# Kernel optimization log

Measured on AMD Instinct MI355X. Metric: run time of the kernel, lower is better.

## Reference

```python
import jax, jax.numpy as jnp
import numpy as np

N, E, IN, ED, H, C = 50000, 800000, 128, 32, 4, 32
HC = H * C
SCALE = 1.0 / float(np.sqrt(C))


def _seg_softmax(t, idx, n):
    # t: [E, H], idx: [E] target-node ids -> per-segment softmax over incoming edges
    m = jax.ops.segment_max(t, idx, num_segments=n)
    m = jnp.where(jnp.isfinite(m), m, 0.0)
    e = jnp.exp(t - m[idx])
    z = jax.ops.segment_sum(e, idx, num_segments=n)
    return e / (z[idx] + 1e-16)


def setup_inputs() -> dict:
    key = jax.random.key(0)
    ks = jax.random.split(key, 26)
    w = lambda k, shape: (jax.random.normal(k, shape, jnp.float32) * 0.05)
    return {
        "x": jax.random.normal(ks[0], (N, IN), jnp.float32),
        "edge_index": jax.random.randint(ks[1], (2, E), 0, N),
        "edge_attr": jax.random.normal(ks[2], (E, ED), jnp.float32),
        # DifferentialGraphAttention params (dual QK groups + lambda)
        "Wq1": w(ks[3], (HC, IN)), "Wq2": w(ks[4], (HC, IN)),
        "Wk1": w(ks[5], (HC, IN)), "Wk2": w(ks[6], (HC, IN)),
        "Wvd": w(ks[7], (HC, IN)),
        "Wkr1": w(ks[8], (HC, ED)), "Wkr2": w(ks[9], (HC, ED)),
        "Wvrd": w(ks[10], (HC, ED)),
        "Woutd": w(ks[11], (HC, HC)),
        "lam": jnp.float32(0.8),
        # RelationActivationAttention params
        "Wqa": w(ks[12], (HC, IN)), "Wka": w(ks[13], (HC, IN)), "Wva": w(ks[14], (HC, IN)),
        "Wkra": w(ks[15], (HC, ED)), "Wvra": w(ks[16], (HC, ED)),
        "Wouta": w(ks[17], (HC, HC)),
        # Hybrid fusion params
        "Wproj": w(ks[18], (HC, 2 * HC)), "bproj": jnp.zeros((HC,), jnp.float32),
        "Win": w(ks[19], (HC, IN)), "b_in": jnp.zeros((HC,), jnp.float32),
        "rms_w": jnp.ones((HC,), jnp.float32),
    }


def reference(x, edge_index, edge_attr, Wq1, Wq2, Wk1, Wk2, Wvd, Wkr1, Wkr2, Wvrd,
              Woutd, lam, Wqa, Wka, Wva, Wkra, Wvra, Wouta, Wproj, bproj, Win, b_in,
              rms_w):
    src, dst = edge_index[0], edge_index[1]

    def nproj(W):  # [N, HC] -> [N, H, C]
        return (x @ W.T).reshape(N, H, C)

    def eproj(W):  # [E, HC] -> [E, H, C]
        return (edge_attr @ W.T).reshape(E, H, C)

    # ---- differential relation aggregation branch ----
    Q1, Q2, K1, K2, Vd = nproj(Wq1), nproj(Wq2), nproj(Wk1), nproj(Wk2), nproj(Wvd)
    t1 = jnp.sum(Q1[dst] * (K1[src] + eproj(Wkr1)), axis=-1) * SCALE  # [E, H]
    t2 = jnp.sum(Q2[dst] * (K2[src] + eproj(Wkr2)), axis=-1) * SCALE
    a_diff = _seg_softmax(t1, dst, N) - lam * _seg_softmax(t2, dst, N)
    msg_d = (Vd[src] + eproj(Wvrd)) * a_diff[..., None]               # [E, H, C]
    h_aggr = jax.ops.segment_sum(msg_d, dst, num_segments=N).reshape(N, HC) @ Woutd.T

    # ---- relation activation branch ----
    Qa, Ka, Va = nproj(Wqa), nproj(Wka), nproj(Wva)
    ta = jnp.sum(Qa[dst] * (Ka[src] + eproj(Wkra)), axis=-1) * SCALE  # [E, H]
    a_act = _seg_softmax(ta, dst, N)
    msg_a = (Va[src] + eproj(Wvra)) * a_act[..., None]
    h_actv = jax.ops.segment_sum(msg_a, dst, num_segments=N).reshape(N, HC) @ Wouta.T

    # ---- hybrid fusion + residual + RMSNorm ----
    h = jnp.concatenate([h_aggr, h_actv], axis=-1) @ Wproj.T + bproj
    h = h + (x @ Win.T + b_in)
    h = h * jax.lax.rsqrt(jnp.mean(h * h, axis=-1, keepdims=True) + 1e-6) * rms_w
    return h
```

## Files before the change

kernel.cpp:

```cpp
#include <hip/hip_runtime.h>

typedef unsigned short u16;
typedef unsigned int   u32;
typedef _Float16 half8 __attribute__((ext_vector_type(8)));
typedef _Float16 half2v __attribute__((ext_vector_type(2)));
typedef float    f32x4 __attribute__((ext_vector_type(4)));
typedef unsigned int u32x4 __attribute__((ext_vector_type(4)));
typedef int      i32x2 __attribute__((ext_vector_type(2)));

#define NN 50000
#define EE 800000
#define SCALE 0.17677669529663687f
#define NB 49

#define O_WNODET   0ul
#define O_WFT      393216ul
#define O_WF1      524288ul
#define O_WF3      589824ul
#define O_HIST     655360ul
#define O_BSUM     855360ul
#define O_BOFF     855616ul
#define O_OFF      856064ul
#define O_CUR      1056768ul
#define O_PERM     1257472ul
#define O_NODEQ    7657472ul
#define O_NODEKV   97257472ul
#define O_G        161257472ul

__device__ __forceinline__ float fin(float x){
  return (x == x && fabsf(x) < 3e38f) ? x : 0.f;
}
__device__ __forceinline__ u32 packh(float a, float b){
  union{ u32 u; _Float16 h[2]; } cv; cv.h[0]=(_Float16)a; cv.h[1]=(_Float16)b; return cv.u;
}
union H2U { u32 u; half2v h; };
__device__ __forceinline__ half2v h2(u32 u){ H2U c; c.u=u; return c.h; }

__device__ __forceinline__ u32x4 ntl4(const u32* p){
  return __builtin_nontemporal_load((const u32x4*)p);
}
__device__ __forceinline__ f32x4 ntlf4(const float* p){
  return __builtin_nontemporal_load((const f32x4*)p);
}
__device__ __forceinline__ i32x2 ntl2(const i32x2* p){
  return __builtin_nontemporal_load(p);
}

__global__ __launch_bounds__(256) void xcast(const float* __restrict__ x,
                                             _Float16* __restrict__ xh,
                                             int* __restrict__ hist, int* __restrict__ cur)
{
  int i = blockIdx.x*256 + threadIdx.x;
  if (i < NN){ hist[i] = 0; cur[i] = 0; }
  size_t b = (size_t)i * 8;
  float4 v0 = *(const float4*)(x + b);
  float4 v1 = *(const float4*)(x + b + 4);
  half8 h;
  h[0]=(_Float16)v0.x; h[1]=(_Float16)v0.y; h[2]=(_Float16)v0.z; h[3]=(_Float16)v0.w;
  h[4]=(_Float16)v1.x; h[5]=(_Float16)v1.y; h[6]=(_Float16)v1.z; h[7]=(_Float16)v1.w;
  *(half8*)(xh + b) = h;
}

__global__ __launch_bounds__(256) void prep1(
    const float* __restrict__ Wq1, const float* __restrict__ Wq2, const float* __restrict__ Wqa,
    const float* __restrict__ Wk1, const float* __restrict__ Wk2, const float* __restrict__ Wka,
    const float* __restrict__ Wvd, const float* __restrict__ Wva, const float* __restrict__ Win,
    const float* __restrict__ Wkr1, const float* __restrict__ Wkr2, const float* __restrict__ Wkra,
    const float* __restrict__ Wproj, const float* __restrict__ Woutd, const float* __restrict__ Wouta,
    _Float16* __restrict__ WnodeT, float* __restrict__ Wf1, float* __restrict__ Wf3)
{
  int job = blockIdx.x*256 + threadIdx.x;
  if (job < 1536*128) {
    int n = job >> 7, kk = job & 127;
    int slot = n >> 7, o = n & 127;
    float val;
    if (slot==3 || slot==4 || slot==5) {
      const float* Wkr = (slot==3)?Wkr1:(slot==4)?Wkr2:Wkra;
      const float* Wq  = (slot==3)?Wq1 :(slot==4)?Wq2 :Wqa;
      int h=o>>5, j=o&31;
      float s=0.f;
      for (int c=0;c<32;c++)
        s += Wkr[(h*32+c)*32 + j] * Wq[(h*32+c)*128 + kk];
      val = s;
    } else {
      const float* W = (slot==0)?Wq1:(slot==1)?Wq2:(slot==2)?Wqa:
                       (slot==6)?Wk1:(slot==7)?Wk2:(slot==8)?Wka:
                       (slot==9)?Wvd:(slot==10)?Wva:Win;
      val = W[o*128 + kk];
    }
    WnodeT[n*128 + kk] = (_Float16)fin(val);
  } else {
    int idx = job - 1536*128;
    int which = idx >> 14;
    int r = idx & 16383;
    int o = r >> 7, v = r & 127;
    const float* Wout = which ? Wouta : Woutd;
    float s=0.f;
    for (int u=0;u<128;u++)
      s += Wproj[o*256 + which*128 + u] * Wout[u*128 + v];
    (which?Wf3:Wf1)[o*128+v] = fin(s);
  }
}

__global__ __launch_bounds__(256) void prep2(
    const float* __restrict__ Wf1, const float* __restrict__ Wf3,
    const float* __restrict__ Wvrd, const float* __restrict__ Wvra,
    _Float16* __restrict__ WfT)
{
  int job = blockIdx.x*256 + threadIdx.x;
  int o = job >> 9, kk = job & 511;
  int seg = kk >> 7, v = kk & 127;
  float val;
  if (seg==0) val = Wf1[o*128+v];
  else if (seg==2) val = Wf3[o*128+v];
  else {
    const float* Wf = (seg==1)?Wf1:Wf3;
    const float* Wv = (seg==1)?Wvrd:Wvra;
    int h=v>>5, j=v&31; float s=0.f;
    for (int c=0;c<32;c++)
      s += Wf[o*128 + h*32 + c] * Wv[(h*32+c)*32 + j];
    val = s;
  }
  WfT[o*512 + kk] = (_Float16)fin(val);
}

__global__ __launch_bounds__(256) void gemm_node(
    const _Float16* __restrict__ xh, const _Float16* __restrict__ WnodeT,
    const float* __restrict__ b_in,
    _Float16* __restrict__ nodeQ, _Float16* __restrict__ nodeKV)
{
  __shared__ _Float16 S[18432];
  _Float16 (*As)[72] = (_Float16(*)[72])S;
  _Float16 (*Bs)[72] = (_Float16(*)[72])(S + 9216);
  int m0 = blockIdx.x * 128;
  int slot = blockIdx.y;
  int n0 = slot * 128;
  int tid = threadIdx.x;
  int lane = tid & 63, wave = tid >> 6;
  int lm = lane & 15, lq = lane >> 4;
  int mbase = wave*32;
  f32x4 acc[2][8];
  #pragma unroll
  for (int i=0;i<2;i++)
    #pragma unroll
    for (int j=0;j<8;j++) acc[i][j] = (f32x4){0.f,0.f,0.f,0.f};

  for (int kt=0; kt<2; kt++){
    int kk0 = kt*64;
    #pragma unroll
    for (int i=0;i<4;i++){
      int c = tid + i*256;
      int row = c >> 3, kc = (c & 7) * 8;
      int grow = m0 + row;
      half8 hv;
      if (grow < NN){
        hv = *(const half8*)(xh + (size_t)grow*128 + kk0 + kc);
      } else {
        #pragma unroll
        for (int j=0;j<8;j++) hv[j] = (_Float16)0.f;
      }
      *(half8*)&As[row][kc] = hv;
      *(half8*)&Bs[row][kc] = *(const half8*)(WnodeT + (size_t)(n0+row)*128 + kk0 + kc);
    }
    __syncthreads();
    #pragma unroll
    for (int ks=0; ks<64; ks+=32){
      half8 a0 = *(half8*)&As[mbase + lm][ks + lq*8];
      half8 a1 = *(half8*)&As[mbase + 16 + lm][ks + lq*8];
      #pragma unroll
      for (int ct=0; ct<8; ct++){
        half8 b = *(half8*)&Bs[ct*16 + lm][ks + lq*8];
        acc[0][ct] = __builtin_amdgcn_mfma_f32_16x16x32_f16(a0, b, acc[0][ct], 0,0,0);
        acc[1][ct] = __builtin_amdgcn_mfma_f32_16x16x32_f16(a1, b, acc[1][ct], 0,0,0);
      }
    }
    __syncthreads();
  }

  #pragma unroll
  for (int rt=0; rt<2; rt++){
    #pragma unroll
    for (int reg=0; reg<4; reg++){
      int row = mbase + rt*16 + lq*4 + reg;
      #pragma unroll
      for (int ct=0; ct<8; ct++){
        int col = ct*16 + lm;
        float bias = (slot == 11) ? b_in[col] : 0.f;
        S[row*136 + col] = (_Float16)fin(acc[rt][ct][reg] + bias);
      }
    }
  }
  __syncthreads();
  #pragma unroll
  for (int i=0;i<8;i++){
    int idx = tid + i*256;
    int row = idx >> 4, c8 = (idx & 15)*8;
    int grow = m0 + row;
    if (grow < NN){
      half8 v = *(half8*)&S[row*136 + c8];
      _Float16* dst = (slot < 6)  ? nodeQ  + (size_t)grow*896 + slot*128 + c8
                    : (slot < 11) ? nodeKV + (size_t)grow*640 + (slot-6)*128 + c8
                                  : nodeQ  + (size_t)grow*896 + 768 + c8;
      *(half8*)dst = v;
    }
  }
}

__global__ __launch_bounds__(256) void hist_k(const int* __restrict__ ei, int* __restrict__ hist){
  int e = blockIdx.x*256 + threadIdx.x;
  int d = ei[EE + e];
  if ((unsigned)d < (unsigned)NN) atomicAdd(&hist[d], 1);
}

__global__ __launch_bounds__(1024) void scan1(const int* __restrict__ hist,
                                              int* __restrict__ loc, int* __restrict__ bsum){
  __shared__ int buf[1024];
  int i = blockIdx.x*1024 + threadIdx.x;
  int v = (i < NN) ? hist[i] : 0;
  buf[threadIdx.x] = v;
  __syncthreads();
  int xv = v;
  for (int s = 1; s < 1024; s <<= 1){
    int t = 0;
    if ((int)threadIdx.x >= s) t = buf[threadIdx.x - s];
    __syncthreads();
    xv += t;
    buf[threadIdx.x] = xv;
    __syncthreads();
  }
  if (i < NN) loc[i] = xv - v;
  if (threadIdx.x == 1023) bsum[blockIdx.x] = xv;
}

__global__ __launch_bounds__(64) void scan2(const int* __restrict__ bsum, int* __restrict__ boff){
  int t = threadIdx.x;
  int v = (t < NB) ? bsum[t] : 0;
  int x = v;
  for (int s = 1; s < 64; s <<= 1){
    int u = __shfl_up(x, s);
    if (t >= s) x += u;
  }
  if (t < NB) boff[t] = x - v;
}

__global__ __launch_bounds__(256) void scatter_k(const int* __restrict__ ei,
                                                 const int* __restrict__ loc, const int* __restrict__ boff,
                                                 int* __restrict__ cur, int2* __restrict__ pe2){
  int e = blockIdx.x*256 + threadIdx.x;
  int d = ei[EE + e];
  if ((unsigned)d >= (unsigned)NN) return;
  int pos = loc[d] + boff[d>>10] + atomicAdd(&cur[d], 1);
  if ((unsigned)pos < (unsigned)EE) pe2[pos] = make_int2(e, ei[e]);
}

__global__ __launch_bounds__(64, 4) void attn_k(
    const i32x2* __restrict__ pe2, const int* __restrict__ hist,
    const int* __restrict__ loc, const int* __restrict__ boff,
    const u32* __restrict__ nfQ, const u32* __restrict__ nfKV,
    const float* __restrict__ ea,
    const float* __restrict__ lamp, u32* __restrict__ G, int nbase)
{
  int lane = threadIdx.x & 63;
  int node = nbase + blockIdx.x;
  if (node >= NN) return;
  int E = lane >> 4;
  int l = lane & 15;
  int h = l >> 2;
  const u32* pd = nfQ + (u32)node * 448u;

  int k = hist[node];
  if (k < 0) k = 0;
  if (k > 64) k = 64;
  int o = loc[node] + boff[node>>10];
  if (o < 0) o = 0;

  int pe_e = 0, pe_s = 0;
  if (k > 0){
    int idxl = (lane < k) ? lane : (k-1);
    i32x2 pl = ntl2(&pe2[o + idxl]);
    pe_e = pl[0]; pe_s = pl[1];
  }

  H2U q1[4], q2[4], qa[4], r1[4], r2[4], ra[4];
  {
    u32x4 a = ntl4(pd +        l*4);
    u32x4 b = ntl4(pd +  64 + l*4);
    u32x4 c = ntl4(pd + 128 + l*4);
    q1[0].u=a[0]; q1[1].u=a[1]; q1[2].u=a[2]; q1[3].u=a[3];
    q2[0].u=b[0]; q2[1].u=b[1]; q2[2].u=b[2]; q2[3].u=b[3];
    qa[0].u=c[0]; qa[1].u=c[1]; qa[2].u=c[2]; qa[3].u=c[3];
    int rb = h*16 + (l&3)*4;
    u32x4 d = ntl4(pd + 192 + rb);
    u32x4 e = ntl4(pd + 256 + rb);
    u32x4 f = ntl4(pd + 320 + rb);
    r1[0].u=d[0]; r1[1].u=d[1]; r1[2].u=d[2]; r1[3].u=d[3];
    r2[0].u=e[0]; r2[1].u=e[1]; r2[2].u=e[2]; r2[3].u=e[3];
    ra[0].u=f[0]; ra[1].u=f[1]; ra[2].u=f[2]; ra[3].u=f[3];
  }

  H2U s1v[4], s2v[4], sav[4], s1e[4], s2e[4], sae[4];
  #pragma unroll
  for (int t=0;t<4;t++){ s1v[t].u=0; s2v[t].u=0; sav[t].u=0; s1e[t].u=0; s2e[t].u=0; sae[t].u=0; }
  float z1=0.f, z2=0.f, za=0.f;

  int iters = (k + 3) >> 2;
  for (int it=0; it<iters; it++){
    int eidx = it*4 + E;
    bool valid = eidx < k;
    int sn = __shfl(pe_s, eidx);
    int ee = __shfl(pe_e, eidx);
    if (!valid){ sn = 0; ee = 0; }
    if ((unsigned)sn >= (unsigned)NN) sn = 0;
    if ((unsigned)ee >= (unsigned)EE) ee = 0;
    const u32* ps = nfKV + (u32)sn * 320u + (u32)(l*4);
    u32x4 K1 = *(const u32x4*)(ps);
    u32x4 K2 = *(const u32x4*)(ps + 64);
    u32x4 KA = *(const u32x4*)(ps + 128);
    u32x4 VD = *(const u32x4*)(ps + 192);
    u32x4 VA = *(const u32x4*)(ps + 256);
    f32x4 ef0 = ntlf4(ea + (size_t)ee*32 + (l&3)*8);
    f32x4 ef1 = ntlf4(ea + (size_t)ee*32 + (l&3)*8 + 4);
    half2v e0 = {(_Float16)ef0[0], (_Float16)ef0[1]};
    half2v e1 = {(_Float16)ef0[2], (_Float16)ef0[3]};
    half2v e2 = {(_Float16)ef1[0], (_Float16)ef1[1]};
    half2v e3 = {(_Float16)ef1[2], (_Float16)ef1[3]};

    half2v p1h = q1[0].h*h2(K1[0]) + q1[1].h*h2(K1[1]) + q1[2].h*h2(K1[2]) + q1[3].h*h2(K1[3])
               + r1[0].h*e0 + r1[1].h*e1 + r1[2].h*e2 + r1[3].h*e3;
    half2v p2h = q2[0].h*h2(K2[0]) + q2[1].h*h2(K2[1]) + q2[2].h*h2(K2[2]) + q2[3].h*h2(K2[3])
               + r2[0].h*e0 + r2[1].h*e1 + r2[2].h*e2 + r2[3].h*e3;
    half2v pah = qa[0].h*h2(KA[0]) + qa[1].h*h2(KA[1]) + qa[2].h*h2(KA[2]) + qa[3].h*h2(KA[3])
               + ra[0].h*e0 + ra[1].h*e1 + ra[2].h*e2 + ra[3].h*e3;

    H2U c1, c2, c3, t;
    c1.h = p1h; c2.h = p2h; c3.h = pah;
    t.u = __shfl_xor(c1.u, 1); c1.h += t.h;
    t.u = __shfl_xor(c2.u, 1); c2.h += t.h;
    t.u = __shfl_xor(c3.u, 1); c3.h += t.h;
    t.u = __shfl_xor(c1.u, 2); c1.h += t.h;
    t.u = __shfl_xor(c2.u, 2); c2.h += t.h;
    t.u = __shfl_xor(c3.u, 2); c3.h += t.h;
    float p1 = (float)c1.h[0] + (float)c1.h[1];
    float p2 = (float)c2.h[0] + (float)c2.h[1];
    float pa = (float)c3.h[0] + (float)c3.h[1];

    float w1 = valid ? __expf(p1*SCALE) : 0.f;
    float w2 = valid ? __expf(p2*SCALE) : 0.f;
    float wa = valid ? __expf(pa*SCALE) : 0.f;
    _Float16 w1f = (_Float16)w1, w2f = (_Float16)w2, waf = (_Float16)wa;
    half2v w1h = {w1f, w1f}, w2h = {w2f, w2f}, wah = {waf, waf};

    s1v[0].h += w1h*h2(VD[0]); s1v[1].h += w1h*h2(VD[1]); s1v[2].h += w1h*h2(VD[2]); s1v[3].h += w1h*h2(VD[3]);
    s2v[0].h += w2h*h2(VD[0]); s2v[1].h += w2h*h2(VD[1]); s2v[2].h += w2h*h2(VD[2]); s2v[3].h += w2h*h2(VD[3]);
    sav[0].h += wah*h2(VA[0]); sav[1].h += wah*h2(VA[1]); sav[2].h += wah*h2(VA[2]); sav[3].h += wah*h2(VA[3]);
    s1e[0].h += w1h*e0; s1e[1].h += w1h*e1; s1e[2].h += w1h*e2; s1e[3].h += w1h*e3;
    s2e[0].h += w2h*e0; s2e[1].h += w2h*e1; s2e[2].h += w2h*e2; s2e[3].h += w2h*e3;
    sae[0].h += wah*e0; sae[1].h += wah*e1; sae[2].h += wah*e2; sae[3].h += wah*e3;
    z1 += w1; z2 += w2; za += wa;
  }

  #pragma unroll
  for (int s=16; s<=32; s<<=1){
    H2U t;
    #pragma unroll
    for (int j=0;j<4;j++){
      t.u = __shfl_xor(s1v[j].u, s); s1v[j].h += t.h;
      t.u = __shfl_xor(s2v[j].u, s); s2v[j].h += t.h;
      t.u = __shfl_xor(sav[j].u, s); sav[j].h += t.h;
      t.u = __shfl_xor(s1e[j].u, s); s1e[j].h += t.h;
      t.u = __shfl_xor(s2e[j].u, s); s2e[j].h += t.h;
      t.u = __shfl_xor(sae[j].u, s); sae[j].h += t.h;
    }
    z1 += __shfl_xor(z1, s); z2 += __shfl_xor(z2, s); za += __shfl_xor(za, s);
  }

  if (E == 0){
    float lamv = lamp[0];
    float i1 = 1.f/(z1+1e-16f), i2 = 1.f/(z2+1e-16f), ia = 1.f/(za+1e-16f);
    u32 gb = (u32)node*256u;
    int rb = h*16 + (l&3)*4;
    #pragma unroll
    for (int t=0;t<4;t++){
      float d0 = fin((float)s1v[t].h[0]*i1 - lamv*((float)s2v[t].h[0]*i2));
      float d1 = fin((float)s1v[t].h[1]*i1 - lamv*((float)s2v[t].h[1]*i2));
      G[gb + l*4 + t] = packh(d0, d1);
      float e0v = fin((float)s1e[t].h[0]*i1 - lamv*((float)s2e[t].h[0]*i2));
      float e1v = fin((float)s1e[t].h[1]*i1 - lamv*((float)s2e[t].h[1]*i2));
      G[gb + 64 + rb + t] = packh(e0v, e1v);
      G[gb + 128 + l*4 + t] = packh(fin((float)sav[t].h[0]*ia), fin((float)sav[t].h[1]*ia));
      G[gb + 192 + rb + t] = packh(fin((float)sae[t].h[0]*ia), fin((float)sae[t].h[1]*ia));
    }
  }
}

__global__ __launch_bounds__(256) void gemm_final(
    const _Float16* __restrict__ Gf, const _Float16* __restrict__ WfT,
    const _Float16* __restrict__ nodeQ,
    const float* __restrict__ bproj, const float* __restrict__ rmsw,
    float* __restrict__ out)
{
  __shared__ char SS[34816];
  _Float16 (*As)[72] = (_Float16(*)[72])SS;
  _Float16 (*Bs)[72] = (_Float16(*)[72])(SS + 9216);
  float* Sf = (float*)SS;
  __shared__ float bS[128], rS[128];
  int m0 = blockIdx.x * 64;
  int tid = threadIdx.x;
  int lane = tid & 63, wave = tid >> 6;
  int lm = lane & 15, lq = lane >> 4;
  int mbase = wave*16;
  if (tid < 128){ bS[tid] = bproj[tid]; rS[tid] = rmsw[tid]; }
  f32x4 acc[8];
  #pragma unroll
  for (int j=0;j<8;j++) acc[j] = (f32x4){0.f,0.f,0.f,0.f};

  for (int kt=0; kt<8; kt++){
    int kk0 = kt*64;
    #pragma unroll
    for (int i=0;i<2;i++){
      int c = tid + i*256;
      int row = c >> 3, kc = (c & 7) * 8;
      int grow = m0 + row;
      half8 av;
      if (grow < NN){
        av = *(const half8*)(Gf + (size_t)grow*512 + kk0 + kc);
      } else {
        #pragma unroll
        for (int j=0;j<8;j++) av[j] = (_Float16)0.f;
      }
      *(half8*)&As[row][kc] = av;
    }
    #pragma unroll
    for (int i=0;i<4;i++){
      int c = tid + i*256;
      int row = c >> 3, kc = (c & 7) * 8;
      *(half8*)&Bs[row][kc] = *(const half8*)(WfT + (size_t)row*512 + kk0 + kc);
    }
    __syncthreads();
    #pragma unroll
    for (int ks=0; ks<64; ks+=32){
      half8 a0 = *(half8*)&As[mbase + lm][ks + lq*8];
      #pragma unroll
      for (int ct=0; ct<8; ct++){
        half8 b = *(half8*)&Bs[ct*16 + lm][ks + lq*8];
        acc[ct] = __builtin_amdgcn_mfma_f32_16x16x32_f16(a0, b, acc[ct], 0,0,0);
      }
    }
    __syncthreads();
  }
  #pragma unroll
  for (int reg=0; reg<4; reg++){
    int rowl = mbase + lq*4 + reg;
    int row = m0 + rowl;
    bool ok = row < NN;
    float vals[8]; float ss = 0.f;
    #pragma unroll
    for (int ct=0; ct<8; ct++){
      int col = ct*16 + lm;
      float R = ok ? (float)nodeQ[(size_t)row*896 + 768 + col] : 0.f;
      float v = fin(acc[ct][reg] + bS[col] + R);
      vals[ct] = v; ss += v*v;
    }
    #pragma unroll
    for (int sh=1; sh<16; sh<<=1) ss += __shfl_xor(ss, sh);
    float rstd = rsqrtf(ss*(1.0f/128.f) + 1e-6f);
    #pragma unroll
    for (int ct=0; ct<8; ct++){
      int col = ct*16 + lm;
      Sf[rowl*132 + col] = fin(vals[ct]*rstd*rS[col]);
    }
  }
  __syncthreads();
  #pragma unroll
  for (int i=0;i<8;i++){
    int idx = tid + i*256;
    int rowl = idx >> 5, c4 = (idx & 31) * 4;
    int grow = m0 + rowl;
    if (grow < NN){
      f32x4 v = *(f32x4*)&Sf[rowl*132 + c4];
      *(f32x4*)(out + (size_t)grow*128 + c4) = v;
    }
  }
}

extern "C" void kernel_launch(void* const* d_in, const int* in_sizes, int n_in,
                              void* d_out, int out_size, void* d_ws, size_t ws_size,
                              hipStream_t stream)
{
  char* w = (char*)d_ws;
  _Float16* WnodeT = (_Float16*)(w + O_WNODET);
  _Float16* WfT    = (_Float16*)(w + O_WFT);
  float*    Wf1    = (float*)(w + O_WF1);
  float*    Wf3    = (float*)(w + O_WF3);
  int*      hist   = (int*)(w + O_HIST);
  int*      bsum   = (int*)(w + O_BSUM);
  int*      boff   = (int*)(w + O_BOFF);
  int*      loc    = (int*)(w + O_OFF);
  int*      cur    = (int*)(w + O_CUR);
  int2*     pe2    = (int2*)(w + O_PERM);
  _Float16* nodeQ  = (_Float16*)(w + O_NODEQ);
  _Float16* nodeKV = (_Float16*)(w + O_NODEKV);
  _Float16* Gf     = (_Float16*)(w + O_G);
  _Float16* xh     = (_Float16*)(w + O_G);

  const float* x     = (const float*)d_in[0];
  const int*   ei    = (const int*)d_in[1];
  const float* ea    = (const float*)d_in[2];
  const float* Wq1   = (const float*)d_in[3];
  const float* Wq2   = (const float*)d_in[4];
  const float* Wk1   = (const float*)d_in[5];
  const float* Wk2   = (const float*)d_in[6];
  const float* Wvd   = (const float*)d_in[7];
  const float* Wkr1  = (const float*)d_in[8];
  const float* Wkr2  = (const float*)d_in[9];
  const float* Wvrd  = (const float*)d_in[10];
  const float* Woutd = (const float*)d_in[11];
  const float* lam   = (const float*)d_in[12];
  const float* Wqa   = (const float*)d_in[13];
  const float* Wka   = (const float*)d_in[14];
  const float* Wva   = (const float*)d_in[15];
  const float* Wkra  = (const float*)d_in[16];
  const float* Wvra  = (const float*)d_in[17];
  const float* Wouta = (const float*)d_in[18];
  const float* Wproj = (const float*)d_in[19];
  const float* bproj = (const float*)d_in[20];
  const float* Win   = (const float*)d_in[21];
  const float* b_in  = (const float*)d_in[22];
  const float* rmsw  = (const float*)d_in[23];

  xcast<<<3125, 256, 0, stream>>>(x, xh, hist, cur);
  prep1<<<896, 256, 0, stream>>>(Wq1,Wq2,Wqa, Wk1,Wk2,Wka, Wvd,Wva,Win,
                                 Wkr1,Wkr2,Wkra, Wproj,Woutd,Wouta,
                                 WnodeT, Wf1, Wf3);
  prep2<<<256, 256, 0, stream>>>(Wf1, Wf3, Wvrd, Wvra, WfT);
  gemm_node<<<dim3(391,12), 256, 0, stream>>>(xh, WnodeT, b_in, nodeQ, nodeKV);
  hist_k<<<3125, 256, 0, stream>>>(ei, hist);
  scan1<<<NB, 1024, 0, stream>>>(hist, loc, bsum);
  scan2<<<1, 64, 0, stream>>>(bsum, boff);
  scatter_k<<<3125, 256, 0, stream>>>(ei, loc, boff, cur, pe2);
  attn_k<<<12500, 64, 0, stream>>>((const i32x2*)pe2, hist, loc, boff, (const u32*)nodeQ,
                                   (const u32*)nodeKV, ea, lam, (u32*)Gf, 0);
  attn_k<<<12500, 64, 0, stream>>>((const i32x2*)pe2, hist, loc, boff, (const u32*)nodeQ,
                                   (const u32*)nodeKV, ea, lam, (u32*)Gf, 12500);
  attn_k<<<12500, 64, 0, stream>>>((const i32x2*)pe2, hist, loc, boff, (const u32*)nodeQ,
                                   (const u32*)nodeKV, ea, lam, (u32*)Gf, 25000);
  attn_k<<<12500, 64, 0, stream>>>((const i32x2*)pe2, hist, loc, boff, (const u32*)nodeQ,
                                   (const u32*)nodeKV, ea, lam, (u32*)Gf, 37500);
  gemm_final<<<782, 256, 0, stream>>>(Gf, WfT, nodeQ, bproj, rmsw, (float*)d_out);
}
```

Measured before the change: 581.5 us.

## Use single-wave direct-load node GEMM and merge attention launches into one

The node projection GEMM moves from 256-thread blocks that stage 128-row tiles in LDS to 64-thread single-wave blocks of 32 rows. These load A and B fragments straight from global memory into MFMA operands and mask out-of-range rows by multiplying with zero. The four chunked attention launches become a single 50000-block launch, which removes launch gaps and tail effects between chunks. The GEMM trades LDS reuse of the weight tile for fewer barriers and more blocks, so it re-reads weights from global and cache more often.

```diff
diff --git a/kernel.cpp b/kernel.cpp
--- a/kernel.cpp
+++ b/kernel.cpp
@@ -124,64 +124,52 @@
   WfT[o*512 + kk] = (_Float16)fin(val);
 }
 
-__global__ __launch_bounds__(256) void gemm_node(
+__global__ __launch_bounds__(64, 4) void gemm_node(
     const _Float16* __restrict__ xh, const _Float16* __restrict__ WnodeT,
     const float* __restrict__ b_in,
     _Float16* __restrict__ nodeQ, _Float16* __restrict__ nodeKV)
 {
-  __shared__ _Float16 S[18432];
-  _Float16 (*As)[72] = (_Float16(*)[72])S;
-  _Float16 (*Bs)[72] = (_Float16(*)[72])(S + 9216);
-  int m0 = blockIdx.x * 128;
+  __shared__ _Float16 S[32*136];
+  int m0 = blockIdx.x * 32;
   int slot = blockIdx.y;
   int n0 = slot * 128;
-  int tid = threadIdx.x;
-  int lane = tid & 63, wave = tid >> 6;
+  int lane = threadIdx.x & 63;
   int lm = lane & 15, lq = lane >> 4;
-  int mbase = wave*32;
+
   f32x4 acc[2][8];
   #pragma unroll
   for (int i=0;i<2;i++)
     #pragma unroll
     for (int j=0;j<8;j++) acc[i][j] = (f32x4){0.f,0.f,0.f,0.f};
 
-  for (int kt=0; kt<2; kt++){
-    int kk0 = kt*64;
-    #pragma unroll
-    for (int i=0;i<4;i++){
-      int c = tid + i*256;
-      int row = c >> 3, kc = (c & 7) * 8;
-      int grow = m0 + row;
-      half8 hv;
-      if (grow < NN){
-        hv = *(const half8*)(xh + (size_t)grow*128 + kk0 + kc);
-      } else {
-        #pragma unroll
-        for (int j=0;j<8;j++) hv[j] = (_Float16)0.f;
-      }
-      *(half8*)&As[row][kc] = hv;
-      *(half8*)&Bs[row][kc] = *(const half8*)(WnodeT + (size_t)(n0+row)*128 + kk0 + kc);
-    }
-    __syncthreads();
-    #pragma unroll
-    for (int ks=0; ks<64; ks+=32){
-      half8 a0 = *(half8*)&As[mbase + lm][ks + lq*8];
-      half8 a1 = *(half8*)&As[mbase + 16 + lm][ks + lq*8];
-      #pragma unroll
-      for (int ct=0; ct<8; ct++){
-        half8 b = *(half8*)&Bs[ct*16 + lm][ks + lq*8];
-        acc[0][ct] = __builtin_amdgcn_mfma_f32_16x16x32_f16(a0, b, acc[0][ct], 0,0,0);
-        acc[1][ct] = __builtin_amdgcn_mfma_f32_16x16x32_f16(a1, b, acc[1][ct], 0,0,0);
-      }
-    }
-    __syncthreads();
+  int r0 = m0 + lm, r1 = m0 + 16 + lm;
+  bool ok0 = r0 < NN, ok1 = r1 < NN;
+  _Float16 zmask0 = ok0 ? (_Float16)1.f : (_Float16)0.f;
+  _Float16 zmask1 = ok1 ? (_Float16)1.f : (_Float16)0.f;
+  const _Float16* pa0 = xh + (size_t)(ok0 ? r0 : 0)*128 + lq*8;
+  const _Float16* pa1 = xh + (size_t)(ok1 ? r1 : 0)*128 + lq*8;
+  const _Float16* pb  = WnodeT + (size_t)(n0 + lm)*128 + lq*8;
+
+  #pragma unroll
+  for (int ks=0; ks<4; ks++){
+    int kk0 = ks*32;
+    half8 a0 = *(const half8*)(pa0 + kk0);
+    half8 a1 = *(const half8*)(pa1 + kk0);
+    #pragma unroll
+    for (int j=0;j<8;j++){ a0[j] = a0[j]*zmask0; a1[j] = a1[j]*zmask1; }
+    #pragma unroll
+    for (int ct=0; ct<8; ct++){
+      half8 b = *(const half8*)(pb + (size_t)ct*16*128 + kk0);
+      acc[0][ct] = __builtin_amdgcn_mfma_f32_16x16x32_f16(a0, b, acc[0][ct], 0,0,0);
+      acc[1][ct] = __builtin_amdgcn_mfma_f32_16x16x32_f16(a1, b, acc[1][ct], 0,0,0);
+    }
   }
 
   #pragma unroll
   for (int rt=0; rt<2; rt++){
     #pragma unroll
     for (int reg=0; reg<4; reg++){
-      int row = mbase + rt*16 + lq*4 + reg;
+      int row = rt*16 + lq*4 + reg;
       #pragma unroll
       for (int ct=0; ct<8; ct++){
         int col = ct*16 + lm;
@@ -193,7 +181,7 @@
   __syncthreads();
   #pragma unroll
   for (int i=0;i<8;i++){
-    int idx = tid + i*256;
+    int idx = (int)threadIdx.x + i*64;
     int row = idx >> 4, c8 = (idx & 15)*8;
     int grow = m0 + row;
     if (grow < NN){
@@ -258,10 +246,10 @@
     const int* __restrict__ loc, const int* __restrict__ boff,
     const u32* __restrict__ nfQ, const u32* __restrict__ nfKV,
     const float* __restrict__ ea,
-    const float* __restrict__ lamp, u32* __restrict__ G, int nbase)
+    const float* __restrict__ lamp, u32* __restrict__ G)
 {
   int lane = threadIdx.x & 63;
-  int node = nbase + blockIdx.x;
+  int node = blockIdx.x;
   if (node >= NN) return;
   int E = lane >> 4;
   int l = lane & 15;
@@ -533,18 +521,12 @@
                                  Wkr1,Wkr2,Wkra, Wproj,Woutd,Wouta,
                                  WnodeT, Wf1, Wf3);
   prep2<<<256, 256, 0, stream>>>(Wf1, Wf3, Wvrd, Wvra, WfT);
-  gemm_node<<<dim3(391,12), 256, 0, stream>>>(xh, WnodeT, b_in, nodeQ, nodeKV);
+  gemm_node<<<dim3(1563,12), 64, 0, stream>>>(xh, WnodeT, b_in, nodeQ, nodeKV);
   hist_k<<<3125, 256, 0, stream>>>(ei, hist);
   scan1<<<NB, 1024, 0, stream>>>(hist, loc, bsum);
   scan2<<<1, 64, 0, stream>>>(bsum, boff);
   scatter_k<<<3125, 256, 0, stream>>>(ei, loc, boff, cur, pe2);
-  attn_k<<<12500, 64, 0, stream>>>((const i32x2*)pe2, hist, loc, boff, (const u32*)nodeQ,
-                                   (const u32*)nodeKV, ea, lam, (u32*)Gf, 0);
-  attn_k<<<12500, 64, 0, stream>>>((const i32x2*)pe2, hist, loc, boff, (const u32*)nodeQ,
-                                   (const u32*)nodeKV, ea, lam, (u32*)Gf, 12500);
-  attn_k<<<12500, 64, 0, stream>>>((const i32x2*)pe2, hist, loc, boff, (const u32*)nodeQ,
-                                   (const u32*)nodeKV, ea, lam, (u32*)Gf, 25000);
-  attn_k<<<12500, 64, 0, stream>>>((const i32x2*)pe2, hist, loc, boff, (const u32*)nodeQ,
-                                   (const u32*)nodeKV, ea, lam, (u32*)Gf, 37500);
+  attn_k<<<50000, 64, 0, stream>>>((const i32x2*)pe2, hist, loc, boff, (const u32*)nodeQ,
+                                   (const u32*)nodeKV, ea, lam, (u32*)Gf);
   gemm_final<<<782, 256, 0, stream>>>(Gf, WfT, nodeQ, bproj, rmsw, (float*)d_out);
 }
```

Result: slower. 593.4 us (+2.0%).
